# Kernel optimization log

Measured on AMD Instinct MI355X. Metric: run time of the kernel, lower is better.

## Reference

```python
import jax, jax.numpy as jnp
import numpy as np

N_TOTAL = 2_000_000   # total particles across all events
N_EVENTS = 20_000     # number of events (segments)
H = 64                # phi/rho hidden width
OUT = 10              # output classes


def _lin(x, W, b):
    # torch nn.Linear: y = x @ W.T + b
    return x @ W.T + b


def setup_inputs() -> dict:
    key = jax.random.key(0)
    ks = jax.random.split(key, 24)
    s = 0.1  # small init scale
    inp = {
        "values": jax.random.normal(ks[0], (N_TOTAL,), dtype=jnp.float32),
        "seg_ids": jnp.sort(jax.random.randint(ks[1], (N_TOTAL,), 0, N_EVENTS)),
        "p1w0": jax.random.normal(ks[2], (H, 1), dtype=jnp.float32) * s,
        "p1b0": jax.random.normal(ks[3], (H,), dtype=jnp.float32) * s,
        "p1w1": jax.random.normal(ks[4], (H, H), dtype=jnp.float32) * s,
        "p1b1": jax.random.normal(ks[5], (H,), dtype=jnp.float32) * s,
        "r1w0": jax.random.normal(ks[6], (H, H), dtype=jnp.float32) * s,
        "r1b0": jax.random.normal(ks[7], (H,), dtype=jnp.float32) * s,
        "r1w1": jax.random.normal(ks[8], (H, H), dtype=jnp.float32) * s,
        "r1b1": jax.random.normal(ks[9], (H,), dtype=jnp.float32) * s,
        "o1w": jax.random.normal(ks[10], (H, H), dtype=jnp.float32) * s,
        "o1b": jax.random.normal(ks[11], (H,), dtype=jnp.float32) * s,
        "p2w0": jax.random.normal(ks[12], (H, H), dtype=jnp.float32) * s,
        "p2b0": jax.random.normal(ks[13], (H,), dtype=jnp.float32) * s,
        "p2w1": jax.random.normal(ks[14], (H, H), dtype=jnp.float32) * s,
        "p2b1": jax.random.normal(ks[15], (H,), dtype=jnp.float32) * s,
        "r2w0": jax.random.normal(ks[16], (H, H), dtype=jnp.float32) * s,
        "r2b0": jax.random.normal(ks[17], (H,), dtype=jnp.float32) * s,
        "r2w1": jax.random.normal(ks[18], (H, H), dtype=jnp.float32) * s,
        "r2b1": jax.random.normal(ks[19], (H,), dtype=jnp.float32) * s,
        "o2w": jax.random.normal(ks[20], (OUT, H), dtype=jnp.float32) * s,
        "o2b": jax.random.normal(ks[21], (OUT,), dtype=jnp.float32) * s,
    }
    return inp


def reference(values, seg_ids, p1w0, p1b0, p1w1, p1b1, r1w0, r1b0, r1w1, r1b1,
              o1w, o1b, p2w0, p2b0, p2w1, p2b1, r2w0, r2b0, r2w1, r2b1, o2w, o2b):
    relu = jax.nn.relu
    # stage 1: phi1 on each scalar particle value -> [N, H]
    h = relu(_lin(values[:, None], p1w0, p1b0))
    h = relu(_lin(h, p1w1, p1b1))
    # jagged sum over particles within each event (the inner deepset sum)
    ev = jax.ops.segment_sum(h, seg_ids, num_segments=N_EVENTS)  # [E, H]
    # rho1 + output linear + activation per event
    ev = relu(_lin(ev, r1w0, r1b0))
    ev = relu(_lin(ev, r1w1, r1b1))
    ev = relu(_lin(ev, o1w, o1b))  # [E, H] (output_size of deepset1 = rho_sizes[-1])
    # stage 2: phi2 per event, sum over all events
    h2 = relu(_lin(ev, p2w0, p2b0))
    h2 = relu(_lin(h2, p2w1, p2b1))
    s2 = jnp.sum(h2, axis=0, keepdims=True)  # [1, H]
    r2 = relu(_lin(s2, r2w0, r2b0))
    r2 = relu(_lin(r2, r2w1, r2b1))
    out = _lin(r2, o2w, o2b)  # [1, OUT]
    return jax.nn.log_softmax(out, axis=1)
```

## Files before the change

kernel.cpp:

```cpp
#include <hip/hip_runtime.h>

#define NT 2000000
#define NE 20000
#define NTILES (NT / 64)

using bf16x8 = __attribute__((ext_vector_type(8))) __bf16;
using bf16x4 = __attribute__((ext_vector_type(4))) __bf16;
using f32x4  = __attribute__((ext_vector_type(4))) float;
using f32x2  = __attribute__((ext_vector_type(2))) float;
using fvec4  = __attribute__((ext_vector_type(4))) float;

__device__ __forceinline__ void load_bsplit(const float* __restrict__ p,
                                            bf16x8& hi, bf16x8& lo) {
    fvec4 a = *(const fvec4*)p;
    fvec4 b = *(const fvec4*)(p + 4);
#pragma unroll
    for (int e = 0; e < 4; e++) {
        float v  = a[e];
        __bf16 h = (__bf16)v;
        hi[e]    = h;
        lo[e]    = (__bf16)(v - (float)h);
        float v2  = b[e];
        __bf16 h2 = (__bf16)v2;
        hi[e + 4] = h2;
        lo[e + 4] = (__bf16)(v2 - (float)h2);
    }
}

__device__ __forceinline__ bf16x8 load_bf8(const float* __restrict__ p) {
    fvec4 a = *(const fvec4*)p;
    fvec4 b = *(const fvec4*)(p + 4);
    bf16x8 r;
#pragma unroll
    for (int e = 0; e < 4; e++) {
        r[e]     = (__bf16)a[e];
        r[e + 4] = (__bf16)b[e];
    }
    return r;
}

__global__ __launch_bounds__(256, 3) void k1_phi1(
    const float* __restrict__ values, const int* __restrict__ seg,
    const float* __restrict__ w0, const float* __restrict__ b0,
    const float* __restrict__ w1, const float* __restrict__ b1,
    float* __restrict__ ev) {
    const int tid = threadIdx.x;
    const int w   = tid >> 6;
    const int l   = tid & 63;
    const int l15 = l & 15;
    const int l4  = l >> 4;

    bf16x8 Bh[2][4];
#pragma unroll
    for (int kf = 0; kf < 2; kf++)
#pragma unroll
        for (int jf = 0; jf < 4; jf++)
            Bh[kf][jf] = load_bf8(w1 + (jf * 16 + l15) * 64 + kf * 32 + l4 * 8);

    f32x2 w0p[2][4], b0p[2][4];
#pragma unroll
    for (int kf = 0; kf < 2; kf++) {
        const int kb = kf * 32 + l4 * 8;
#pragma unroll
        for (int e2 = 0; e2 < 4; e2++) {
            w0p[kf][e2] = *(const f32x2*)(w0 + kb + e2 * 2);
            b0p[kf][e2] = *(const f32x2*)(b0 + kb + e2 * 2);
        }
    }
    float biasj[4];
#pragma unroll
    for (int jf = 0; jf < 4; jf++) biasj[jf] = b1[jf * 16 + l15];

    for (int tile = blockIdx.x * 4 + w; tile < NTILES; tile += gridDim.x * 4) {
        const int base = tile * 64;
        const int s_l  = seg[base + l];
        const int prev = __shfl_up(s_l, 1);
        const unsigned long long bmask = __ballot((l > 0) && (s_l != prev));

        float vp[4];
#pragma unroll
        for (int pf = 0; pf < 4; pf++) vp[pf] = values[base + pf * 16 + l15];

#pragma unroll
        for (int q = 0; q < 2; q++) {
            f32x4 acc[2][4];
#pragma unroll
            for (int i = 0; i < 2; i++)
#pragma unroll
                for (int jf = 0; jf < 4; jf++)
#pragma unroll
                    for (int r = 0; r < 4; r++) acc[i][jf][r] = biasj[jf];

#pragma unroll
            for (int kf = 0; kf < 2; kf++) {
                bf16x8 A[2];
#pragma unroll
                for (int i = 0; i < 2; i++) {
                    const float vq = vp[2 * q + i];
                    const f32x2 vv = {vq, vq};
#pragma unroll
                    for (int e2 = 0; e2 < 4; e2++) {
                        f32x2 h = w0p[kf][e2] * vv + b0p[kf][e2];
                        A[i][2 * e2]     = (__bf16)fmaxf(h[0], 0.f);
                        A[i][2 * e2 + 1] = (__bf16)fmaxf(h[1], 0.f);
                    }
                }
#pragma unroll
                for (int i = 0; i < 2; i++)
#pragma unroll
                    for (int jf = 0; jf < 4; jf++)
                        acc[i][jf] = __builtin_amdgcn_mfma_f32_16x16x32_bf16(
                            A[i], Bh[kf][jf], acc[i][jf], 0, 0, 0);
            }

#pragma unroll
            for (int i = 0; i < 2; i++)
#pragma unroll
                for (int jf = 0; jf < 4; jf++)
#pragma unroll
                    for (int r = 0; r < 4; r++)
                        acc[i][jf][r] = fmaxf(acc[i][jf][r], 0.f);

            const unsigned int mq =
                (unsigned int)(bmask >> (q * 32)) & 0xFFFFFFFEu;

            if (mq == 0u) {
                const int sid = __builtin_amdgcn_readlane(s_l, q * 32);
                float sj[4];
#pragma unroll
                for (int jf = 0; jf < 4; jf++) {
                    f32x4 t = acc[0][jf] + acc[1][jf];
                    float h = (t[0] + t[1]) + (t[2] + t[3]);
                    h += __shfl_xor(h, 16);
                    h += __shfl_xor(h, 32);
                    sj[jf] = h;
                }
                float v = (l4 == 0) ? sj[0] : (l4 == 1) ? sj[1]
                        : (l4 == 2) ? sj[2] : sj[3];
                atomicAdd(ev + (size_t)sid * 64 + l, v);
            } else {
                unsigned int m = mq;
                int start = 0;
                int sid   = __builtin_amdgcn_readlane(s_l, q * 32);
                while (true) {
                    const int end = m ? (int)__builtin_ctz(m) : 32;
                    float sj[4] = {0.f, 0.f, 0.f, 0.f};
#pragma unroll
                    for (int i = 0; i < 2; i++)
#pragma unroll
                        for (int r = 0; r < 4; r++) {
                            const int rel = i * 16 + l4 * 4 + r;
                            const float pm = (rel >= start && rel < end) ? 1.f : 0.f;
#pragma unroll
                            for (int jf = 0; jf < 4; jf++)
                                sj[jf] = fmaf(acc[i][jf][r], pm, sj[jf]);
                        }
#pragma unroll
                    for (int jf = 0; jf < 4; jf++) {
                        sj[jf] += __shfl_xor(sj[jf], 16);
                        sj[jf] += __shfl_xor(sj[jf], 32);
                    }
                    float v = (l4 == 0) ? sj[0] : (l4 == 1) ? sj[1]
                            : (l4 == 2) ? sj[2] : sj[3];
                    atomicAdd(ev + (size_t)sid * 64 + l, v);
                    if (!m) break;
                    start = end;
                    sid   = __builtin_amdgcn_readlane(s_l, q * 32 + start);
                    m &= (m - 1);
                }
            }
        }
    }
}

__global__ __launch_bounds__(64) void k2_events(
    const float* __restrict__ ev,
    const float* __restrict__ W0, const float* __restrict__ B0,
    const float* __restrict__ W1, const float* __restrict__ B1,
    const float* __restrict__ W2, const float* __restrict__ B2,
    const float* __restrict__ W3, const float* __restrict__ B3,
    const float* __restrict__ W4, const float* __restrict__ B4,
    float* __restrict__ s2) {
    __shared__ __align__(16) __bf16 xt[64 * 72];
    const int l   = threadIdx.x;
    const int l15 = l & 15;
    const int l4  = l >> 4;
    const int ebase = blockIdx.x * 64;

    const float* Ws[5] = {W0, W1, W2, W3, W4};
    const float* Bs[5] = {B0, B1, B2, B3, B4};

    bf16x8 A[4][2];
#pragma unroll
    for (int pf = 0; pf < 4; pf++) {
        const int e = ebase + pf * 16 + l15;
#pragma unroll
        for (int kf = 0; kf < 2; kf++) {
            bf16x8 a;
            if (e < NE) {
                const float* p = ev + (size_t)e * 64 + kf * 32 + l4 * 8;
                fvec4 x = *(const fvec4*)p;
                fvec4 y = *(const fvec4*)(p + 4);
#pragma unroll
                for (int e2 = 0; e2 < 4; e2++) {
                    a[e2]     = (__bf16)x[e2];
                    a[e2 + 4] = (__bf16)y[e2];
                }
            } else {
#pragma unroll
                for (int e2 = 0; e2 < 8; e2++) a[e2] = (__bf16)0.f;
            }
            A[pf][kf] = a;
        }
    }

#pragma unroll
    for (int L = 0; L < 5; L++) {
        bf16x8 Bh[2][4], Bl[2][4];
#pragma unroll
        for (int kf = 0; kf < 2; kf++)
#pragma unroll
            for (int jf = 0; jf < 4; jf++)
                load_bsplit(Ws[L] + (jf * 16 + l15) * 64 + kf * 32 + l4 * 8,
                            Bh[kf][jf], Bl[kf][jf]);

        f32x4 acc[4][4];
#pragma unroll
        for (int jf = 0; jf < 4; jf++) {
            const float bj = Bs[L][jf * 16 + l15];
#pragma unroll
            for (int pf = 0; pf < 4; pf++)
#pragma unroll
                for (int r = 0; r < 4; r++) acc[pf][jf][r] = bj;
        }
#pragma unroll
        for (int kf = 0; kf < 2; kf++)
#pragma unroll
            for (int pf = 0; pf < 4; pf++)
#pragma unroll
                for (int jf = 0; jf < 4; jf++)
                    acc[pf][jf] = __builtin_amdgcn_mfma_f32_16x16x32_bf16(
                        A[pf][kf], Bh[kf][jf], acc[pf][jf], 0, 0, 0);
#pragma unroll
        for (int kf = 0; kf < 2; kf++)
#pragma unroll
            for (int pf = 0; pf < 4; pf++)
#pragma unroll
                for (int jf = 0; jf < 4; jf++)
                    acc[pf][jf] = __builtin_amdgcn_mfma_f32_16x16x32_bf16(
                        A[pf][kf], Bl[kf][jf], acc[pf][jf], 0, 0, 0);

        if (L < 4) {
#pragma unroll
            for (int pf = 0; pf < 4; pf++)
#pragma unroll
                for (int jf = 0; jf < 4; jf++) {
                    const int j = jf * 16 + l15;
#pragma unroll
                    for (int r = 0; r < 4; r++)
                        xt[(pf * 16 + l4 * 4 + r) * 72 + j] =
                            (__bf16)fmaxf(acc[pf][jf][r], 0.f);
                }
#pragma unroll
            for (int pf = 0; pf < 4; pf++)
#pragma unroll
                for (int kf = 0; kf < 2; kf++)
                    A[pf][kf] = *(const bf16x8*)(xt + (pf * 16 + l15) * 72 +
                                                 kf * 32 + l4 * 8);
        } else {
            float sj[4];
#pragma unroll
            for (int jf = 0; jf < 4; jf++) {
                float s = 0.f;
#pragma unroll
                for (int pf = 0; pf < 4; pf++)
#pragma unroll
                    for (int r = 0; r < 4; r++) {
                        const int e = ebase + pf * 16 + l4 * 4 + r;
                        float v = fmaxf(acc[pf][jf][r], 0.f);
                        s += (e < NE) ? v : 0.f;
                    }
                s += __shfl_xor(s, 16);
                s += __shfl_xor(s, 32);
                sj[jf] = s;
            }
            float v = (l4 == 0) ? sj[0] : (l4 == 1) ? sj[1]
                    : (l4 == 2) ? sj[2] : sj[3];
            atomicAdd(s2 + l, v);
        }
    }
}

__global__ __launch_bounds__(64) void k3_final(
    const float* __restrict__ s2,
    const float* __restrict__ W0, const float* __restrict__ B0,
    const float* __restrict__ W1, const float* __restrict__ B1,
    const float* __restrict__ W2, const float* __restrict__ B2,
    float* __restrict__ out) {
    __shared__ __align__(16) float xb[64];
    __shared__ __align__(16) float yb[64];
    __shared__ float ob[10];
    const int l = threadIdx.x;

    xb[l] = s2[l];
    __syncthreads();

    float a = B0[l];
#pragma unroll
    for (int k = 0; k < 16; k++) {
        fvec4 wv = *(const fvec4*)(W0 + l * 64 + k * 4);
        fvec4 xv = *(const fvec4*)(xb + k * 4);
        a += wv[0] * xv[0] + wv[1] * xv[1] + wv[2] * xv[2] + wv[3] * xv[3];
    }
    yb[l] = fmaxf(a, 0.f);
    __syncthreads();

    float b_ = B1[l];
#pragma unroll
    for (int k = 0; k < 16; k++) {
        fvec4 wv = *(const fvec4*)(W1 + l * 64 + k * 4);
        fvec4 xv = *(const fvec4*)(yb + k * 4);
        b_ += wv[0] * xv[0] + wv[1] * xv[1] + wv[2] * xv[2] + wv[3] * xv[3];
    }
    __syncthreads();
    xb[l] = fmaxf(b_, 0.f);
    __syncthreads();

    if (l < 10) {
        float o = B2[l];
#pragma unroll
        for (int k = 0; k < 16; k++) {
            fvec4 wv = *(const fvec4*)(W2 + l * 64 + k * 4);
            fvec4 xv = *(const fvec4*)(xb + k * 4);
            o += wv[0] * xv[0] + wv[1] * xv[1] + wv[2] * xv[2] + wv[3] * xv[3];
        }
        ob[l] = o;
    }
    __syncthreads();
    if (l == 0) {
        float m = ob[0];
#pragma unroll
        for (int i = 1; i < 10; i++) m = fmaxf(m, ob[i]);
        float sum = 0.f;
#pragma unroll
        for (int i = 0; i < 10; i++) sum = sum + expf(ob[i] - m);
        float ls = logf(sum);
#pragma unroll
        for (int i = 0; i < 10; i++) out[i] = ob[i] - m - ls;
    }
}

extern "C" void kernel_launch(void* const* d_in, const int* in_sizes, int n_in,
                              void* d_out, int out_size, void* d_ws, size_t ws_size,
                              hipStream_t stream) {
    const float* values = (const float*)d_in[0];
    const int*   seg    = (const int*)d_in[1];
    const float* p1w0 = (const float*)d_in[2],  *p1b0 = (const float*)d_in[3];
    const float* p1w1 = (const float*)d_in[4],  *p1b1 = (const float*)d_in[5];
    const float* r1w0 = (const float*)d_in[6],  *r1b0 = (const float*)d_in[7];
    const float* r1w1 = (const float*)d_in[8],  *r1b1 = (const float*)d_in[9];
    const float* o1w  = (const float*)d_in[10], *o1b  = (const float*)d_in[11];
    const float* p2w0 = (const float*)d_in[12], *p2b0 = (const float*)d_in[13];
    const float* p2w1 = (const float*)d_in[14], *p2b1 = (const float*)d_in[15];
    const float* r2w0 = (const float*)d_in[16], *r2b0 = (const float*)d_in[17];
    const float* r2w1 = (const float*)d_in[18], *r2b1 = (const float*)d_in[19];
    const float* o2w  = (const float*)d_in[20], *o2b  = (const float*)d_in[21];

    float* ev = (float*)d_ws;
    float* s2 = ev + (size_t)NE * 64;

    hipMemsetAsync(d_ws, 0, (size_t)(NE * 64 + 64) * sizeof(float), stream);

    hipLaunchKernelGGL(k1_phi1, dim3(2048), dim3(256), 0, stream,
                       values, seg, p1w0, p1b0, p1w1, p1b1, ev);
    hipLaunchKernelGGL(k2_events, dim3((NE + 63) / 64), dim3(64), 0, stream,
                       ev, r1w0, r1b0, r1w1, r1b1, o1w, o1b,
                       p2w0, p2b0, p2w1, p2b1, s2);
    hipLaunchKernelGGL(k3_final, dim3(1), dim3(64), 0, stream,
                       s2, r2w0, r2b0, r2w1, r2b1, o2w, o2b, (float*)d_out);
}
```

Baseline: 75.00 us.

## Prefetch next tile, move phi1 layer-0 weights to LDS, cheaper cross-lane reduce

The phi1 kernel now software-pipelines the tile loop, loading the next tile's segment ids and values while the current tile is computed. The layer-0 weights and biases move from registers into shared memory to free VGPRs, and launch bounds rise to 4 waves-per-EU with half as many blocks. The four-column butterfly reduction is replaced by a transposed exchange that needs 3 shuffles instead of 8. The cost is extra LDS reads in the inner loop and more live registers for the prefetched data.

```diff
diff --git a/kernel.cpp b/kernel.cpp
--- a/kernel.cpp
+++ b/kernel.cpp
@@ -39,17 +39,25 @@
     return r;
 }
 
-__global__ __launch_bounds__(256, 3) void k1_phi1(
+__global__ __launch_bounds__(256, 4) void k1_phi1(
     const float* __restrict__ values, const int* __restrict__ seg,
     const float* __restrict__ w0, const float* __restrict__ b0,
     const float* __restrict__ w1, const float* __restrict__ b1,
     float* __restrict__ ev) {
+    __shared__ __align__(16) float lw0[64];
+    __shared__ __align__(16) float lb0[64];
+
     const int tid = threadIdx.x;
     const int w   = tid >> 6;
     const int l   = tid & 63;
     const int l15 = l & 15;
     const int l4  = l >> 4;
 
+    if (tid < 64) {
+        lw0[tid] = w0[tid];
+        lb0[tid] = b0[tid];
+    }
+
     bf16x8 Bh[2][4];
 #pragma unroll
     for (int kf = 0; kf < 2; kf++)
@@ -57,29 +65,47 @@
         for (int jf = 0; jf < 4; jf++)
             Bh[kf][jf] = load_bf8(w1 + (jf * 16 + l15) * 64 + kf * 32 + l4 * 8);
 
-    f32x2 w0p[2][4], b0p[2][4];
-#pragma unroll
-    for (int kf = 0; kf < 2; kf++) {
-        const int kb = kf * 32 + l4 * 8;
-#pragma unroll
-        for (int e2 = 0; e2 < 4; e2++) {
-            w0p[kf][e2] = *(const f32x2*)(w0 + kb + e2 * 2);
-            b0p[kf][e2] = *(const f32x2*)(b0 + kb + e2 * 2);
-        }
-    }
     float biasj[4];
 #pragma unroll
     for (int jf = 0; jf < 4; jf++) biasj[jf] = b1[jf * 16 + l15];
 
-    for (int tile = blockIdx.x * 4 + w; tile < NTILES; tile += gridDim.x * 4) {
-        const int base = tile * 64;
-        const int s_l  = seg[base + l];
-        const int prev = __shfl_up(s_l, 1);
-        const unsigned long long bmask = __ballot((l > 0) && (s_l != prev));
-
-        float vp[4];
-#pragma unroll
-        for (int pf = 0; pf < 4; pf++) vp[pf] = values[base + pf * 16 + l15];
+    __syncthreads();
+
+    const bool bit0 = (l & 16) != 0;
+    const bool bit1 = (l & 32) != 0;
+    auto reduce4 = [&](const float sj[4]) -> float {
+        float send01 = bit0 ? sj[0] : sj[1];
+        float keep01 = bit0 ? sj[1] : sj[0];
+        float c01 = keep01 + __shfl_xor(send01, 16);
+        float send23 = bit0 ? sj[2] : sj[3];
+        float keep23 = bit0 ? sj[3] : sj[2];
+        float c23 = keep23 + __shfl_xor(send23, 16);
+        float send = bit1 ? c01 : c23;
+        float keep = bit1 ? c23 : c01;
+        return keep + __shfl_xor(send, 32);
+    };
+
+    const int stride = gridDim.x * 4;
+    int tile = blockIdx.x * 4 + w;
+
+    int s_cur = seg[tile * 64 + l];
+    float vp[4];
+#pragma unroll
+    for (int pf = 0; pf < 4; pf++) vp[pf] = values[tile * 64 + pf * 16 + l15];
+
+    while (tile < NTILES) {
+        const int ntile = tile + stride;
+        int s_nxt = 0;
+        float vpn[4] = {0.f, 0.f, 0.f, 0.f};
+        if (ntile < NTILES) {
+            const int nb = ntile * 64;
+            s_nxt = seg[nb + l];
+#pragma unroll
+            for (int pf = 0; pf < 4; pf++) vpn[pf] = values[nb + pf * 16 + l15];
+        }
+
+        const int prev = __shfl_up(s_cur, 1);
+        const unsigned long long bmask = __ballot((l > 0) && (s_cur != prev));
 
 #pragma unroll
         for (int q = 0; q < 2; q++) {
@@ -93,16 +119,23 @@
 
 #pragma unroll
             for (int kf = 0; kf < 2; kf++) {
+                const float* wk = lw0 + kf * 32 + l4 * 8;
+                const float* bk = lb0 + kf * 32 + l4 * 8;
+                const fvec4 wa = *(const fvec4*)wk;
+                const fvec4 wb = *(const fvec4*)(wk + 4);
+                const fvec4 ba = *(const fvec4*)bk;
+                const fvec4 bb = *(const fvec4*)(bk + 4);
+
                 bf16x8 A[2];
 #pragma unroll
                 for (int i = 0; i < 2; i++) {
                     const float vq = vp[2 * q + i];
-                    const f32x2 vv = {vq, vq};
-#pragma unroll
-                    for (int e2 = 0; e2 < 4; e2++) {
-                        f32x2 h = w0p[kf][e2] * vv + b0p[kf][e2];
-                        A[i][2 * e2]     = (__bf16)fmaxf(h[0], 0.f);
-                        A[i][2 * e2 + 1] = (__bf16)fmaxf(h[1], 0.f);
+#pragma unroll
+                    for (int e = 0; e < 4; e++) {
+                        float h0 = fmaxf(fmaf(vq, wa[e], ba[e]), 0.f);
+                        float h1 = fmaxf(fmaf(vq, wb[e], bb[e]), 0.f);
+                        A[i][e]     = (__bf16)h0;
+                        A[i][e + 4] = (__bf16)h1;
                     }
                 }
 #pragma unroll
@@ -125,23 +158,18 @@
                 (unsigned int)(bmask >> (q * 32)) & 0xFFFFFFFEu;
 
             if (mq == 0u) {
-                const int sid = __builtin_amdgcn_readlane(s_l, q * 32);
+                const int sid = __builtin_amdgcn_readlane(s_cur, q * 32);
                 float sj[4];
 #pragma unroll
                 for (int jf = 0; jf < 4; jf++) {
                     f32x4 t = acc[0][jf] + acc[1][jf];
-                    float h = (t[0] + t[1]) + (t[2] + t[3]);
-                    h += __shfl_xor(h, 16);
-                    h += __shfl_xor(h, 32);
-                    sj[jf] = h;
+                    sj[jf] = (t[0] + t[1]) + (t[2] + t[3]);
                 }
-                float v = (l4 == 0) ? sj[0] : (l4 == 1) ? sj[1]
-                        : (l4 == 2) ? sj[2] : sj[3];
-                atomicAdd(ev + (size_t)sid * 64 + l, v);
+                atomicAdd(ev + (size_t)sid * 64 + l, reduce4(sj));
             } else {
                 unsigned int m = mq;
                 int start = 0;
-                int sid   = __builtin_amdgcn_readlane(s_l, q * 32);
+                int sid   = __builtin_amdgcn_readlane(s_cur, q * 32);
                 while (true) {
                     const int end = m ? (int)__builtin_ctz(m) : 32;
                     float sj[4] = {0.f, 0.f, 0.f, 0.f};
@@ -155,21 +183,19 @@
                             for (int jf = 0; jf < 4; jf++)
                                 sj[jf] = fmaf(acc[i][jf][r], pm, sj[jf]);
                         }
-#pragma unroll
-                    for (int jf = 0; jf < 4; jf++) {
-                        sj[jf] += __shfl_xor(sj[jf], 16);
-                        sj[jf] += __shfl_xor(sj[jf], 32);
-                    }
-                    float v = (l4 == 0) ? sj[0] : (l4 == 1) ? sj[1]
-                            : (l4 == 2) ? sj[2] : sj[3];
-                    atomicAdd(ev + (size_t)sid * 64 + l, v);
+                    atomicAdd(ev + (size_t)sid * 64 + l, reduce4(sj));
                     if (!m) break;
                     start = end;
-                    sid   = __builtin_amdgcn_readlane(s_l, q * 32 + start);
+                    sid   = __builtin_amdgcn_readlane(s_cur, q * 32 + start);
                     m &= (m - 1);
                 }
             }
         }
+
+        tile  = ntile;
+        s_cur = s_nxt;
+#pragma unroll
+        for (int pf = 0; pf < 4; pf++) vp[pf] = vpn[pf];
     }
 }
 
@@ -371,7 +397,7 @@
 
     hipMemsetAsync(d_ws, 0, (size_t)(NE * 64 + 64) * sizeof(float), stream);
 
-    hipLaunchKernelGGL(k1_phi1, dim3(2048), dim3(256), 0, stream,
+    hipLaunchKernelGGL(k1_phi1, dim3(1024), dim3(256), 0, stream,
                        values, seg, p1w0, p1b0, p1w1, p1b1, ev);
     hipLaunchKernelGGL(k2_events, dim3((NE + 63) / 64), dim3(64), 0, stream,
                        ev, r1w0, r1b0, r1w1, r1b1, o1w, o1b,
```

After: 152.5 us. 103% more time.
